# Optimization experiments

Measured on AMD Instinct MI355X. Metric: run time of the kernel, lower is better.

The kernel has to match this reference:

```python
import jax, jax.numpy as jnp
import numpy as np

HIDDEN = 768
MLP = 4 * HIDDEN

def layernorm(x, g, b, eps=1e-5):
    mu = jnp.mean(x, axis=-1, keepdims=True)
    var = jnp.var(x, axis=-1, keepdims=True)
    return (x - mu) * jax.lax.rsqrt(var + eps) * g + b

def setup_inputs() -> dict:
    key = jax.random.key(0)
    ks = jax.random.split(key, 10)
    b, l, h = 8, 1024, HIDDEN
    s = 1.0 / np.sqrt(h)
    inp = {
        "x": jax.random.normal(ks[0], (b, l, h), dtype=jnp.float32),
        "Wq": jax.random.normal(ks[1], (h, h), dtype=jnp.float32) * s,
        "Wk": jax.random.normal(ks[2], (h, h), dtype=jnp.float32) * s,
        "Wv": jax.random.normal(ks[3], (h, h), dtype=jnp.float32) * s,
        "Wo": jax.random.normal(ks[4], (h, h), dtype=jnp.float32) * s,
        "W1": jax.random.normal(ks[5], (h, MLP), dtype=jnp.float32) * s,
        "b1": jnp.zeros((MLP,), dtype=jnp.float32),
        "W2": jax.random.normal(ks[6], (MLP, h), dtype=jnp.float32) * (1.0 / np.sqrt(MLP)),
        "b2": jnp.zeros((h,), dtype=jnp.float32),
        "g1": jnp.ones((h,), dtype=jnp.float32),
        "be1": jnp.zeros((h,), dtype=jnp.float32),
        "g2": jnp.ones((h,), dtype=jnp.float32),
        "be2": jnp.zeros((h,), dtype=jnp.float32),
        "n_heads": 12,
    }
    return inp

def reference(x, Wq, Wk, Wv, Wo, W1, b1, W2, b2, g1, be1, g2, be2, n_heads):
    b, l, h = x.shape
    d = h // n_heads
    # NOTE: faithful to source — heads are the LAST axis of a plain reshape,
    # and the second einsum contracts with K (not V), reproducing the original code.
    q = (x @ Wq).reshape(b, l, d, n_heads)
    k = (x @ Wk).reshape(b, l, d, n_heads)
    v = (x @ Wv).reshape(b, l, d, n_heads)  # computed but unused downstream, as in source
    scores = jnp.einsum('bldn,bmdn->blmn', q, k) / (d ** 0.5)
    attn = jax.nn.softmax(scores, axis=2)  # softmax over m (dim=2), as in source
    ctx = jnp.einsum('blmn,bmdn->bldn', attn, k).reshape(b, l, h)
    attn_out = ctx @ Wo
    x = x + attn_out
    x = layernorm(x, g1, be1)
    ff = (jax.nn.gelu(x @ W1 + b1, approximate=False) @ W2) + b2
    x = x + ff
    x = layernorm(x, g2, be2)
    return x
```

## Files before the change

### kernel.cpp

```cpp
#include <hip/hip_runtime.h>
#include <math.h>

typedef unsigned short u16;
typedef unsigned int u32;
typedef short bf16x8 __attribute__((ext_vector_type(8)));
typedef float f32x4 __attribute__((ext_vector_type(4)));

#define MFMA(a, b, c) __builtin_amdgcn_mfma_f32_16x16x32_bf16((a), (b), (c), 0, 0, 0)

#define GLOAD_LDS16(g, l)                                                              \
    __builtin_amdgcn_global_load_lds((const __attribute__((address_space(1))) void*)(g), \
                                     (__attribute__((address_space(3))) void*)(l), 16, 0, 0)

__device__ __forceinline__ u16 f2bf(float f) {
    u32 u = __float_as_uint(f);
    u32 r = (u + 0x7fffu + ((u >> 16) & 1u)) >> 16;
    return (u16)r;
}

__device__ __forceinline__ float fast_gelu(float z) {
    float u = fminf(1.5957691216f * z * (1.0f + 0.044715f * z * z), 80.0f);
    float e = __expf(u);
    float r = __builtin_amdgcn_rcpf(e + 1.0f);
    return z * e * r;
}

__device__ void dev_xcast(const float* __restrict__ in, u16* __restrict__ out, int blk) {
    size_t i = ((size_t)blk * 256 + threadIdx.x) * 8;
    const float4* p = reinterpret_cast<const float4*>(in + i);
    float4 a = p[0], b = p[1];
    union { u16 u[8]; uint4 v; } o;
    o.u[0] = f2bf(a.x); o.u[1] = f2bf(a.y); o.u[2] = f2bf(a.z); o.u[3] = f2bf(a.w);
    o.u[4] = f2bf(b.x); o.u[5] = f2bf(b.y); o.u[6] = f2bf(b.z); o.u[7] = f2bf(b.w);
    *reinterpret_cast<uint4*>(out + i) = o.v;
}

__device__ void dev_transpose(const float* __restrict__ in, u16* __restrict__ out,
                              int K, int N, int bx, int by, float* tile ) {
    int k0 = by * 64, n0 = bx * 64;
    int t = threadIdx.x;
    for (int p = 0; p < 16; p++) {
        int idx = t + p * 256;
        int r = idx >> 6, c = idx & 63;
        tile[r * 65 + c] = in[(size_t)(k0 + r) * N + n0 + c];
    }
    __syncthreads();
    for (int p = 0; p < 16; p++) {
        int idx = t + p * 256;
        int nr = idx >> 6, nc = idx & 63;
        out[(size_t)(n0 + nr) * K + k0 + nc] = f2bf(tile[nc * 65 + nr]);
    }
}

__device__ void dev_wo(const float* __restrict__ in, u16* __restrict__ out,
                       int bx, int by, float* tile ) {
    int k0 = by * 96, n0 = bx * 64;
    int t = threadIdx.x;
    for (int p = 0; p < 24; p++) {
        int idx = t + p * 256;
        int r = idx >> 6, c = idx & 63;
        tile[r * 65 + c] = in[(size_t)(k0 + r) * 768 + n0 + c];
    }
    __syncthreads();
    for (int p = 0; p < 3; p++) {
        int idx = t + p * 256;
        int c = idx / 12, n = idx % 12;
        union { u16 u[8]; uint4 v; } o;
        for (int j = 0; j < 8; j++) o.u[j] = f2bf(tile[(j * 12 + n) * 65 + c]);
        *reinterpret_cast<uint4*>(&out[(size_t)(n0 + c) * 768 + n * 64 + by * 8]) = o.v;
    }
}

__global__ __launch_bounds__(256) void prep_k(const float* __restrict__ x,
                                              const float* __restrict__ Wq,
                                              const float* __restrict__ Wk,
                                              const float* __restrict__ Wo,
                                              const float* __restrict__ W1,
                                              const float* __restrict__ W2,
                                              u16* __restrict__ XB,
                                              u16* __restrict__ WQKT,
                                              u16* __restrict__ WOT,
                                              u16* __restrict__ W1T,
                                              u16* __restrict__ W2T) {
    __shared__ float tile[96 * 65];
    int bid = blockIdx.x;
    if (bid < 3072) {
        dev_xcast(x, XB, bid);
    } else if (bid < 3216) {
        int b = bid - 3072; dev_transpose(Wq, WQKT, 768, 768, b % 12, b / 12, tile);
    } else if (bid < 3360) {
        int b = bid - 3216; dev_transpose(Wk, WQKT + (size_t)768 * 768, 768, 768, b % 12, b / 12, tile);
    } else if (bid < 3456) {
        int b = bid - 3360; dev_wo(Wo, WOT, b % 12, b / 12, tile);
    } else if (bid < 4032) {
        int b = bid - 3456; dev_transpose(W1, W1T, 768, 3072, b % 48, b / 48, tile);
    } else {
        int b = bid - 4032; dev_transpose(W2, W2T, 3072, 768, b % 12, b / 12, tile);
    }
}

template <int EPI, int TM, bool AH = false>
__global__ __launch_bounds__(256) void gemm_bt_k(const u16* __restrict__ A,
                                                 const u16* __restrict__ BT,
                                                 int M, int N, int K, int NBX,
                                                 float* __restrict__ outF,
                                                 u16* __restrict__ outB,
                                                 const float* __restrict__ resid,
                                                 const float* __restrict__ bias) {
    constexpr int MI = TM / 32;
    constexpr int NS = (TM == 64) ? 4 : 3;
    __shared__ __align__(16) u16 As[NS][TM * 32];
    __shared__ __align__(16) u16 Bs[NS][128 * 32];

    int L = blockIdx.x;
    int bx = (L >> 3) % NBX;
    int by = (L / (8 * NBX)) * 8 + (L & 7);
    int m0 = by * TM, n0 = bx * 128;

    int t = threadIdx.x;
    int wave = t >> 6, lane = t & 63;
    int wr = (wave >> 1) * (TM / 2), wc = (wave & 1) * 64;
    int ln = lane & 15, quad = lane >> 4;
    int sw = quad ^ ((ln >> 1) & 3);

    int e0 = t, e1 = t + 256;
    int r0 = e0 >> 2, c0 = (e0 & 3) ^ ((r0 >> 1) & 3);
    int r1 = e1 >> 2, c1 = (e1 & 3) ^ ((r1 >> 1) & 3);
    const u16* A0 = A + (size_t)(m0 + r0) * K + c0 * 8;
    const u16* A1 = A + (size_t)(m0 + r1) * K + c1 * 8;
    const u16* B0 = BT + (size_t)(n0 + r0) * K + c0 * 8;
    const u16* B1 = BT + (size_t)(n0 + r1) * K + c1 * 8;
    const u16* Abase = nullptr;
    if constexpr (AH) {
        int m = m0 + r0;
        Abase = A + ((size_t)(m >> 10) * 12288 + (m & 1023)) * 64;
    }

    int nk = K >> 5;

    f32x4 acc[MI][4];
    for (int i = 0; i < MI; i++)
        for (int j = 0; j < 4; j++)
            for (int r = 0; r < 4; r++) acc[i][j][r] = 0.0f;

    for (int s = 0; s < NS - 1; s++) {
        if constexpr (AH) {
            int col8 = s * 4 + c0;
            GLOAD_LDS16(Abase + (col8 >> 3) * 65536 + (col8 & 7) * 8, &As[s][e0 * 8]);
        } else {
            GLOAD_LDS16(A0 + s * 32, &As[s][e0 * 8]);
            if constexpr (TM == 128) GLOAD_LDS16(A1 + s * 32, &As[s][e1 * 8]);
        }
        GLOAD_LDS16(B0 + s * 32, &Bs[s][e0 * 8]);
        GLOAD_LDS16(B1 + s * 32, &Bs[s][e1 * 8]);
    }

    for (int k = 0; k < nk; k++) {
        if constexpr (TM == 64) asm volatile("s_waitcnt vmcnt(6)" ::: "memory");
        else                    asm volatile("s_waitcnt vmcnt(4)" ::: "memory");
        asm volatile("s_barrier" ::: "memory");
        {
            int ks = k + NS - 1 < nk ? k + NS - 1 : nk - 1;
            int bi = (k + NS - 1) % NS;
            if constexpr (AH) {
                int col8 = ks * 4 + c0;
                GLOAD_LDS16(Abase + (col8 >> 3) * 65536 + (col8 & 7) * 8, &As[bi][e0 * 8]);
            } else {
                GLOAD_LDS16(A0 + ks * 32, &As[bi][e0 * 8]);
                if constexpr (TM == 128) GLOAD_LDS16(A1 + ks * 32, &As[bi][e1 * 8]);
            }
            GLOAD_LDS16(B0 + ks * 32, &Bs[bi][e0 * 8]);
            GLOAD_LDS16(B1 + ks * 32, &Bs[bi][e1 * 8]);
        }
        const u16* as = As[k % NS];
        const u16* bs = Bs[k % NS];
        bf16x8 afr[MI], bfr[4];
        for (int i = 0; i < MI; i++)
            afr[i] = *reinterpret_cast<const bf16x8*>(&as[(wr + i * 16 + ln) * 32 + sw * 8]);
        for (int j = 0; j < 4; j++)
            bfr[j] = *reinterpret_cast<const bf16x8*>(&bs[(wc + j * 16 + ln) * 32 + sw * 8]);
        for (int i = 0; i < MI; i++)
            for (int j = 0; j < 4; j++)
                acc[i][j] = MFMA(afr[i], bfr[j], acc[i][j]);
    }

    for (int i = 0; i < MI; i++) {
        for (int j = 0; j < 4; j++) {
            int col = n0 + wc + j * 16 + ln;
            if constexpr (EPI == 4) {
                bool isQ = col < 768;
                int cc = isQ ? col : col - 768;
                int n = cc % 12, d = cc / 12;
                float scl = isQ ? 0.125f : 1.0f;
                u16* base = outB + (isQ ? 0 : 6291456) + (size_t)n * 65536 + d;
                for (int r = 0; r < 4; r++) {
                    int row = m0 + wr + i * 16 + quad * 4 + r;
                    base[(size_t)(row >> 10) * 786432 + (size_t)(row & 1023) * 64] =
                        f2bf(acc[i][j][r] * scl);
                }
            } else {
                for (int r = 0; r < 4; r++) {
                    int row = m0 + wr + i * 16 + quad * 4 + r;
                    size_t idx = (size_t)row * N + col;
                    float v = acc[i][j][r];
                    if constexpr (EPI == 1) {
                        outF[idx] = resid[idx] + v;
                    } else if constexpr (EPI == 2) {
                        outB[idx] = f2bf(fast_gelu(v + bias[col]));
                    } else if constexpr (EPI == 3) {
                        outF[idx] = resid[idx] + v + bias[col];
                    }
                }
            }
        }
    }
}

__global__ __launch_bounds__(256) void attention_k(const u16* __restrict__ QH,
                                                   const u16* __restrict__ KH,
                                                   u16* __restrict__ CTXH) {
    __shared__ __align__(16) u16 Ks[64 * 72];
    __shared__ __align__(16) u16 KsT[64 * 72];
    __shared__ __align__(16) u16 Pl[4][16 * 64];
    int bh = blockIdx.y;
    int l0 = blockIdx.x * 64;
    int t = threadIdx.x, wave = t >> 6, lane = t & 63;
    int ln = lane & 15, quad = lane >> 4;
    int lw = l0 + wave * 16;

    const u16* qrow = QH + (size_t)bh * 65536 + (size_t)(lw + ln) * 64;
    bf16x8 a0 = *reinterpret_cast<const bf16x8*>(qrow + quad * 8);
    bf16x8 a1 = *reinterpret_cast<const bf16x8*>(qrow + 32 + quad * 8);

    f32x4 o[4];
    for (int dt = 0; dt < 4; dt++)
        for (int r = 0; r < 4; r++) o[dt][r] = 0.0f;
    float lst[4];
    for (int r = 0; r < 4; r++) lst[r] = 0.0f;

    const u16* Kbase = KH + (size_t)bh * 65536;
    int mi = t & 63, ds = (t >> 6) * 16;
    int psw = (ln >> 2) & 3;

    union { u16 u[8]; uint4 v; } kva, kvb;
    kva.v = *reinterpret_cast<const uint4*>(&Kbase[(size_t)mi * 64 + ds]);
    kvb.v = *reinterpret_cast<const uint4*>(&Kbase[(size_t)mi * 64 + ds + 8]);

    for (int mb = 0; mb < 16; mb++) {
        __syncthreads();
        *reinterpret_cast<uint4*>(&Ks[mi * 72 + ds]) = kva.v;
        *reinterpret_cast<uint4*>(&Ks[mi * 72 + ds + 8]) = kvb.v;
        for (int j = 0; j < 8; j++) KsT[(ds + j) * 72 + mi] = kva.u[j];
        for (int j = 0; j < 8; j++) KsT[(ds + 8 + j) * 72 + mi] = kvb.u[j];
        __syncthreads();

        {
            int mnext = (mb + 1 < 16 ? mb + 1 : 15) * 64;
            kva.v = *reinterpret_cast<const uint4*>(&Kbase[(size_t)(mnext + mi) * 64 + ds]);
            kvb.v = *reinterpret_cast<const uint4*>(&Kbase[(size_t)(mnext + mi) * 64 + ds + 8]);
        }

        f32x4 st[4];
        for (int nt = 0; nt < 4; nt++) {
            bf16x8 bk0 = *reinterpret_cast<bf16x8*>(&Ks[(nt * 16 + ln) * 72 + quad * 8]);
            bf16x8 bk1 = *reinterpret_cast<bf16x8*>(&Ks[(nt * 16 + ln) * 72 + 32 + quad * 8]);
            f32x4 z;
            for (int r = 0; r < 4; r++) z[r] = 0.0f;
            z = MFMA(a0, bk0, z);
            st[nt] = MFMA(a1, bk1, z);
        }

        for (int r = 0; r < 4; r++) {
            int row = quad * 4 + r;
            float psum = 0.0f;
            for (int nt = 0; nt < 4; nt++) {
                float p = __expf(fminf(st[nt][r], 30.0f));
                psum += p;
                Pl[wave][row * 64 + (((nt * 2 + (ln >> 3)) ^ quad) * 8) + (ln & 7)] = f2bf(p);
            }
            lst[r] += psum;
        }

        bf16x8 pf0 = *reinterpret_cast<bf16x8*>(&Pl[wave][ln * 64 + (quad ^ psw) * 8]);
        bf16x8 pf1 = *reinterpret_cast<bf16x8*>(&Pl[wave][ln * 64 + (quad ^ psw) * 8 + 32]);
        for (int dt = 0; dt < 4; dt++) {
            bf16x8 bk0 = *reinterpret_cast<bf16x8*>(&KsT[(dt * 16 + ln) * 72 + quad * 8]);
            bf16x8 bk1 = *reinterpret_cast<bf16x8*>(&KsT[(dt * 16 + ln) * 72 + 32 + quad * 8]);
            o[dt] = MFMA(pf0, bk0, o[dt]);
            o[dt] = MFMA(pf1, bk1, o[dt]);
        }
    }

    for (int r = 0; r < 4; r++)
        for (int off = 1; off < 16; off <<= 1) lst[r] += __shfl_xor(lst[r], off, 64);

    u16* out = CTXH + (size_t)bh * 65536;
    for (int r = 0; r < 4; r++) {
        float inv = 1.0f / lst[r];
        int row = lw + quad * 4 + r;
        for (int dt = 0; dt < 4; dt++)
            out[(size_t)row * 64 + dt * 16 + ln] = f2bf(o[dt][r] * inv);
    }
}

__global__ __launch_bounds__(256) void layernorm_k(const float* __restrict__ in,
                                                   float* __restrict__ outF,
                                                   u16* __restrict__ outB,
                                                   const float* __restrict__ g,
                                                   const float* __restrict__ be) {
    __shared__ float red[8];
    int row = blockIdx.x;
    int t = threadIdx.x;
    const float* p = in + (size_t)row * 768;
    float v0 = p[t], v1 = p[t + 256], v2 = p[t + 512];
    float s = v0 + v1 + v2;
    float ss = v0 * v0 + v1 * v1 + v2 * v2;
    for (int off = 32; off >= 1; off >>= 1) {
        s += __shfl_xor(s, off, 64);
        ss += __shfl_xor(ss, off, 64);
    }
    int wave = t >> 6, lane = t & 63;
    if (lane == 0) { red[wave] = s; red[4 + wave] = ss; }
    __syncthreads();
    float S = red[0] + red[1] + red[2] + red[3];
    float SS = red[4] + red[5] + red[6] + red[7];
    float mean = S * (1.0f / 768.0f);
    float var = SS * (1.0f / 768.0f) - mean * mean;
    float rstd = rsqrtf(var + 1e-5f);
    float o0 = (v0 - mean) * rstd * g[t] + be[t];
    float o1 = (v1 - mean) * rstd * g[t + 256] + be[t + 256];
    float o2 = (v2 - mean) * rstd * g[t + 512] + be[t + 512];
    float* q = outF + (size_t)row * 768;
    q[t] = o0; q[t + 256] = o1; q[t + 512] = o2;
    if (outB) {
        u16* qb = outB + (size_t)row * 768;
        qb[t] = f2bf(o0); qb[t + 256] = f2bf(o1); qb[t + 512] = f2bf(o2);
    }
}

extern "C" void kernel_launch(void* const* d_in, const int* in_sizes, int n_in,
                              void* d_out, int out_size, void* d_ws, size_t ws_size,
                              hipStream_t stream) {
    const float* x   = (const float*)d_in[0];
    const float* Wq  = (const float*)d_in[1];
    const float* Wk  = (const float*)d_in[2];
    const float* Wo  = (const float*)d_in[4];
    const float* W1  = (const float*)d_in[5];
    const float* b1  = (const float*)d_in[6];
    const float* W2  = (const float*)d_in[7];
    const float* b2  = (const float*)d_in[8];
    const float* g1  = (const float*)d_in[9];
    const float* be1 = (const float*)d_in[10];
    const float* g2  = (const float*)d_in[11];
    const float* be2 = (const float*)d_in[12];
    float* out = (float*)d_out;

    const int S = 8192, H = 768, MLP4 = 3072, H2 = 1536;

    char* ws = (char*)d_ws;
    u16* XB   = (u16*)ws;  ws += (size_t)S * H * 2;
    u16* WQKT = (u16*)ws;  ws += (size_t)H2 * H * 2;
    u16* WOT  = (u16*)ws;  ws += (size_t)H * H * 2;
    u16* W1T  = (u16*)ws;  ws += (size_t)H * MLP4 * 2;
    u16* W2T  = (u16*)ws;  ws += (size_t)H * MLP4 * 2;
    u16* QKH  = (u16*)ws;  ws += (size_t)S * H2 * 2;
    float* Y  = (float*)ws; ws += (size_t)S * H * 4;
    u16* HB   = (u16*)ws;  ws += (size_t)S * MLP4 * 2;

    u16* CTXH = XB;
    u16* X1B  = QKH;

    prep_k<<<4608, 256, 0, stream>>>(x, Wq, Wk, Wo, W1, W2, XB, WQKT, WOT, W1T, W2T);

    gemm_bt_k<4, 128><<<12 * 64, 256, 0, stream>>>(XB, WQKT, S, H2, H, 12, nullptr, QKH, nullptr, nullptr);

    attention_k<<<dim3(16, 96), 256, 0, stream>>>(QKH, QKH + (size_t)S * H, CTXH);

    gemm_bt_k<1, 64, true><<<6 * 128, 256, 0, stream>>>(CTXH, WOT, S, H, H, 6, Y, nullptr, x, nullptr);
    layernorm_k<<<S, 256, 0, stream>>>(Y, Y, X1B, g1, be1);

    gemm_bt_k<2, 128><<<24 * 64, 256, 0, stream>>>(X1B, W1T, S, MLP4, H, 24, nullptr, HB, nullptr, b1);
    gemm_bt_k<3, 64><<<6 * 128, 256, 0, stream>>>(HB, W2T, S, H, MLP4, 6, Y, nullptr, Y, b2);
    layernorm_k<<<S, 256, 0, stream>>>(Y, out, nullptr, g2, be2);
}
```

Before: 424.7 us.

## Write QK GEMM output row-major and repack K per head in separate kernel

The QK projection GEMM now writes its output in plain row-major layout instead of scattering each element into a per-head layout, which removes the strided 2-byte stores from the epilogue. A new head_pack kernel transposes only the K half into the head-major layout through shared memory. Attention now reads Q directly from the row-major buffer with strided scalar gathers. This adds an extra kernel launch and a read and write of K, and makes the Q loads in attention uncoalesced.

```diff
diff --git a/kernel.cpp b/kernel.cpp
--- a/kernel.cpp
+++ b/kernel.cpp
@@ -99,6 +99,28 @@
     }
 }
 
+__global__ __launch_bounds__(256) void head_pack_k(const u16* __restrict__ in, int ld,
+                                                   u16* __restrict__ out) {
+    __shared__ u16 tile[16 * 768];
+    int b = blockIdx.y;
+    int l0 = blockIdx.x * 16;
+    int t = threadIdx.x;
+    for (int p = 0; p < 6; p++) {
+        int c = t + p * 256;
+        int li = c / 96, dc = c % 96;
+        *reinterpret_cast<uint4*>(&tile[li * 768 + dc * 8]) =
+            *reinterpret_cast<const uint4*>(&in[(size_t)(b * 1024 + l0 + li) * ld + dc * 8]);
+    }
+    __syncthreads();
+    for (int p = 0; p < 6; p++) {
+        int c = t + p * 256;
+        int n = c >> 7, rem = c & 127, li = rem >> 3, k8 = rem & 7;
+        union { u16 u[8]; uint4 v; } o;
+        for (int j = 0; j < 8; j++) o.u[j] = tile[li * 768 + (k8 * 8 + j) * 12 + n];
+        *reinterpret_cast<uint4*>(&out[(size_t)((b * 12 + n) * 1024 + l0 + li) * 64 + k8 * 8]) = o.v;
+    }
+}
+
 template <int EPI, int TM, bool AH = false>
 __global__ __launch_bounds__(256) void gemm_bt_k(const u16* __restrict__ A,
                                                  const u16* __restrict__ BT,
@@ -187,50 +209,47 @@
     for (int i = 0; i < MI; i++) {
         for (int j = 0; j < 4; j++) {
             int col = n0 + wc + j * 16 + ln;
-            if constexpr (EPI == 4) {
-                bool isQ = col < 768;
-                int cc = isQ ? col : col - 768;
-                int n = cc % 12, d = cc / 12;
-                float scl = isQ ? 0.125f : 1.0f;
-                u16* base = outB + (isQ ? 0 : 6291456) + (size_t)n * 65536 + d;
-                for (int r = 0; r < 4; r++) {
-                    int row = m0 + wr + i * 16 + quad * 4 + r;
-                    base[(size_t)(row >> 10) * 786432 + (size_t)(row & 1023) * 64] =
-                        f2bf(acc[i][j][r] * scl);
-                }
-            } else {
-                for (int r = 0; r < 4; r++) {
-                    int row = m0 + wr + i * 16 + quad * 4 + r;
-                    size_t idx = (size_t)row * N + col;
-                    float v = acc[i][j][r];
-                    if constexpr (EPI == 1) {
-                        outF[idx] = resid[idx] + v;
-                    } else if constexpr (EPI == 2) {
-                        outB[idx] = f2bf(fast_gelu(v + bias[col]));
-                    } else if constexpr (EPI == 3) {
-                        outF[idx] = resid[idx] + v + bias[col];
-                    }
+            for (int r = 0; r < 4; r++) {
+                int row = m0 + wr + i * 16 + quad * 4 + r;
+                size_t idx = (size_t)row * N + col;
+                float v = acc[i][j][r];
+                if constexpr (EPI == 1) {
+                    outF[idx] = resid[idx] + v;
+                } else if constexpr (EPI == 2) {
+                    outB[idx] = f2bf(fast_gelu(v + bias[col]));
+                } else if constexpr (EPI == 3) {
+                    outF[idx] = resid[idx] + v + bias[col];
+                } else {
+                    outB[idx] = f2bf(col < 768 ? v * 0.125f : v);
                 }
             }
         }
     }
 }
 
-__global__ __launch_bounds__(256) void attention_k(const u16* __restrict__ QH,
+__global__ __launch_bounds__(256) void attention_k(const u16* __restrict__ QB, int ldq,
                                                    const u16* __restrict__ KH,
                                                    u16* __restrict__ CTXH) {
     __shared__ __align__(16) u16 Ks[64 * 72];
     __shared__ __align__(16) u16 KsT[64 * 72];
     __shared__ __align__(16) u16 Pl[4][16 * 64];
     int bh = blockIdx.y;
+    int b = bh / 12, n = bh % 12;
     int l0 = blockIdx.x * 64;
     int t = threadIdx.x, wave = t >> 6, lane = t & 63;
     int ln = lane & 15, quad = lane >> 4;
     int lw = l0 + wave * 16;
 
-    const u16* qrow = QH + (size_t)bh * 65536 + (size_t)(lw + ln) * 64;
-    bf16x8 a0 = *reinterpret_cast<const bf16x8*>(qrow + quad * 8);
-    bf16x8 a1 = *reinterpret_cast<const bf16x8*>(qrow + 32 + quad * 8);
+    bf16x8 a0, a1;
+    {
+        union { u16 u[8]; bf16x8 v; } q0, q1;
+        const u16* qrow = QB + (size_t)(b * 1024 + lw + ln) * ldq + n;
+        for (int j = 0; j < 8; j++) {
+            q0.u[j] = qrow[(quad * 8 + j) * 12];
+            q1.u[j] = qrow[(32 + quad * 8 + j) * 12];
+        }
+        a0 = q0.v; a1 = q1.v;
+    }
 
     f32x4 o[4];
     for (int dt = 0; dt < 4; dt++)
@@ -363,18 +382,20 @@
     u16* WOT  = (u16*)ws;  ws += (size_t)H * H * 2;
     u16* W1T  = (u16*)ws;  ws += (size_t)H * MLP4 * 2;
     u16* W2T  = (u16*)ws;  ws += (size_t)H * MLP4 * 2;
-    u16* QKH  = (u16*)ws;  ws += (size_t)S * H2 * 2;
+    u16* QKB  = (u16*)ws;  ws += (size_t)S * H2 * 2;
+    u16* KH   = (u16*)ws;  ws += (size_t)S * H * 2;
     float* Y  = (float*)ws; ws += (size_t)S * H * 4;
     u16* HB   = (u16*)ws;  ws += (size_t)S * MLP4 * 2;
 
     u16* CTXH = XB;
-    u16* X1B  = QKH;
+    u16* X1B  = QKB;
 
     prep_k<<<4608, 256, 0, stream>>>(x, Wq, Wk, Wo, W1, W2, XB, WQKT, WOT, W1T, W2T);
 
-    gemm_bt_k<4, 128><<<12 * 64, 256, 0, stream>>>(XB, WQKT, S, H2, H, 12, nullptr, QKH, nullptr, nullptr);
-
-    attention_k<<<dim3(16, 96), 256, 0, stream>>>(QKH, QKH + (size_t)S * H, CTXH);
+    gemm_bt_k<4, 128><<<12 * 64, 256, 0, stream>>>(XB, WQKT, S, H2, H, 12, nullptr, QKB, nullptr, nullptr);
+
+    head_pack_k<<<dim3(64, 8), 256, 0, stream>>>(QKB + H, H2, KH);
+    attention_k<<<dim3(16, 96), 256, 0, stream>>>(QKB, H2, KH, CTXH);
 
     gemm_bt_k<1, 64, true><<<6 * 128, 256, 0, stream>>>(CTXH, WOT, S, H, H, 6, Y, nullptr, x, nullptr);
     layernorm_k<<<S, 256, 0, stream>>>(Y, Y, X1B, g1, be1);
```

Result: faster. 404.0 us (-4.9%).
